# Performance work log

Hardware: AMD Instinct MI355X
Metric: run time of the kernel (lower is better)

Reference implementation:

```python
import jax, jax.numpy as jnp
import numpy as np

C = 512
B, Q, H, W = 4, 4, 64, 64


def setup_inputs() -> dict:
    key = jax.random.key(0)
    ks = jax.random.split(key, 16)
    s = 1.0 / np.sqrt(C)
    sb = 1.0 / np.sqrt(C // 4)
    return {
        "x1": jax.random.normal(ks[0], (B, C, Q, H, W), jnp.float32),
        "x2": jax.random.normal(ks[1], (B, C, Q, H, W), jnp.float32),
        "Wq": jax.random.normal(ks[2], (C, C), jnp.float32) * s,
        "bq": jnp.zeros((C,), jnp.float32),
        "Wk": jax.random.normal(ks[3], (C, C), jnp.float32) * s,
        "bk": jnp.zeros((C,), jnp.float32),
        "Wv": jax.random.normal(ks[4], (C, C), jnp.float32) * s,
        "bv": jnp.zeros((C,), jnp.float32),
        "Wa1": jax.random.normal(ks[5], (C // 4, C), jnp.float32) * s,
        "ba1": jnp.zeros((C // 4,), jnp.float32),
        "Wa2": jax.random.normal(ks[6], (4, C // 4), jnp.float32) * sb,
        "ba2": jnp.zeros((4,), jnp.float32),
        "Wo": jax.random.normal(ks[7], (C, C), jnp.float32) * s,
        "bo": jnp.zeros((C,), jnp.float32),
        "gamma": jnp.ones((C,), jnp.float32),
        "beta": jnp.zeros((C,), jnp.float32),
    }


def _conv1x1(x, Wt, b):
    # shared 1x1 conv applied independently to each quaternion component
    # x: [B, Cin, Q, H, W] -> [B, Cout, Q, H, W]
    return jnp.einsum("oc,bcqhw->boqhw", Wt, x) + b[None, :, None, None, None]


def reference(x1, x2, Wq, bq, Wk, bk, Wv, bv, Wa1, ba1, Wa2, ba2, Wo, bo, gamma, beta):
    Bn, Cn, Qn, Hn, Wn = x1.shape
    G = Cn // 4  # head dim / channel groups
    q = _conv1x1(x1, Wq, bq)
    k = _conv1x1(x2, Wk, bk)
    v = _conv1x1(x2, Wv, bv)
    # angle gate: C -> C//4 -> relu -> 4, softmax over the 4 gate channels
    aw = jax.nn.softmax(_conv1x1(jax.nn.relu(_conv1x1(x1, Wa1, ba1)), Wa2, ba2), axis=1)  # [B,4,Q,H,W]
    def gate(t):
        return (t.reshape(Bn, G, 4, Qn, Hn, Wn) * aw[:, None]).reshape(Bn, Cn, Qn, Hn, Wn)
    q = gate(q)
    k = gate(k)
    S = Qn * Hn * Wn
    def heads(t):
        # [B,C,Q,H,W] -> [B, 4 heads, G, S]
        return t.reshape(Bn, G, 4, S).transpose(0, 2, 1, 3)
    qh, kh, vh = heads(q), heads(k), heads(v)
    scale = 1.0 / jnp.sqrt(jnp.asarray(G, qh.dtype))
    attn = jax.nn.softmax(jnp.einsum("bhgs,bhfs->bhgf", qh, kh) * scale, axis=-1)  # [B,4,G,G]
    out = jnp.einsum("bhgf,bhfs->bhgs", attn, vh)  # [B,4,G,S]
    out = out.transpose(0, 2, 1, 3).reshape(Bn, Cn, Qn, Hn, Wn)
    out = _conv1x1(out, Wo, bo)
    # IQBN: normalize each (channel, quaternion component) over (B,H,W)
    mean = out.mean(axis=(0, 3, 4), keepdims=True)
    var = out.var(axis=(0, 3, 4), keepdims=True)
    out = (out - mean) / jnp.sqrt(var + 1e-5)
    return out * gamma[None, :, None, None, None] + beta[None, :, None, None, None]
```

## Files before the change

### kernel.cpp

```cpp
#include <hip/hip_runtime.h>


#define DEVI __device__ __forceinline__
typedef unsigned short u16;
typedef __bf16 bf16x8 __attribute__((ext_vector_type(8)));
typedef float f32x4 __attribute__((ext_vector_type(4)));

DEVI float bf2f(unsigned int u) {
  union { unsigned int u; float f; } v; v.u = u << 16; return v.f;
}
DEVI u16 f2bf(float f) {
  union { float f; unsigned int u; } v; v.f = f;
  unsigned int r = v.u + 0x7FFFu + ((v.u >> 16) & 1u);
  return (u16)(r >> 16);
}
DEVI void gload_lds16(const void* gp, void* lp) {
  __builtin_amdgcn_global_load_lds((const __attribute__((address_space(1))) int*)gp,
                                   (__attribute__((address_space(3))) int*)lp, 16, 0, 0);
}

__global__ __launch_bounds__(256) void cvtW_k(const float* __restrict__ Wq, const float* __restrict__ Wk,
                                              const float* __restrict__ Wa1, u16* __restrict__ WQB,
                                              u16* __restrict__ WKB, u16* __restrict__ WA1B) {
  int i = blockIdx.x * 256 + threadIdx.x;
  const float* src; u16* dst; int off;
  if (i < 65536) { src = Wq; dst = WQB; off = i; }
  else if (i < 131072) { src = Wk; dst = WKB; off = i - 65536; }
  else { src = Wa1; dst = WA1B; off = i - 131072; }
  float4 v = reinterpret_cast<const float4*>(src)[off];
  ushort4 o; o.x = f2bf(v.x); o.y = f2bf(v.y); o.z = f2bf(v.z); o.w = f2bf(v.w);
  reinterpret_cast<ushort4*>(dst)[off] = o;
}

__global__ __launch_bounds__(256) void transpose_cvt(const float* __restrict__ in, u16* __restrict__ out,
                                                     int R, int Cc, long sIn, long sOut) {
  __shared__ float tile[64][65];
  const int t = threadIdx.x;
  const int c0 = blockIdx.x * 64, r0 = blockIdx.y * 64, b = blockIdx.z;
  const float* ip = in + (long)b * sIn;
  u16* op = out + (long)b * sOut;
#pragma unroll
  for (int i = 0; i < 4; ++i) {
    int r = (t >> 4) + i * 16;
    int c = (t & 15) * 4;
    float4 v = *reinterpret_cast<const float4*>(ip + (long)(r0 + r) * Cc + c0 + c);
    tile[r][c] = v.x; tile[r][c + 1] = v.y; tile[r][c + 2] = v.z; tile[r][c + 3] = v.w;
  }
  __syncthreads();
#pragma unroll
  for (int i = 0; i < 4; ++i) {
    int c = (t >> 4) + i * 16;
    int r = (t & 15) * 4;
    ushort4 o;
    o.x = f2bf(tile[r][c]); o.y = f2bf(tile[r + 1][c]);
    o.z = f2bf(tile[r + 2][c]); o.w = f2bf(tile[r + 3][c]);
    *reinterpret_cast<ushort4*>(op + (long)(c0 + c) * R + r0 + r) = o;
  }
}

__global__ __launch_bounds__(256) void woh_k(const float* __restrict__ Wo, u16* __restrict__ Woh) {
  int idx = blockIdx.x * 256 + threadIdx.x;
  int h = idx >> 16;
  int o = (idx >> 7) & 511;
  int g = idx & 127;
  union { float f; unsigned int u; } v; v.f = Wo[(long)o * 512 + 4 * g + h];
  unsigned int r = v.u + 0x7FFFu + ((v.u >> 16) & 1u);
  Woh[idx] = (u16)(r >> 16);
}

enum { MODE_GATE = 0, MODE_BIAS = 1, MODE_PLAIN = 2, MODE_FOLD1 = 3 };

template <int MODE>
__global__ __launch_bounds__(256) void gemm_bt(const u16* __restrict__ A, const u16* __restrict__ Bt,
                                               u16* __restrict__ C, const float* __restrict__ bias,
                                               const float* __restrict__ aw, float* __restrict__ stata,
                                               int M, int N, int K, long sA, long sB, long sC) {
  __shared__ union {
    struct { u16 As[128 * 64]; u16 Bs[128 * 64]; } st;
    float racc[128][2];
  } sm;
  const int t = threadIdx.x;
  const int bn = blockIdx.x, bm = blockIdx.y, bz = blockIdx.z;
  const u16* Ab; const u16* Bb;
  if constexpr (MODE == MODE_FOLD1) {
    Ab = A + (long)(bz & 3) * 512 * 128;
    Bb = Bt + (long)bz * 128 * 128;
  } else {
    Ab = A + (long)bz * sA;
    Bb = Bt + (long)bz * sB;
  }
  const u16* Atile = Ab + (long)(bm * 128) * K;
  const u16* Btile = Bb + (long)(bn * 128) * K;
  const int wid = t >> 6, l = t & 63;
  const int rbase = (wid >> 1) * 64, cbase = (wid & 1) * 64;
  const int lr = l & 15, hi = l >> 4;
  f32x4 acc[4][4] = {};
  for (int kt = 0; kt < K; kt += 64) {
#pragma unroll
    for (int i = 0; i < 4; ++i) {
      int idx = t + i * 256;
      int r = idx >> 3;
      int gs = ((idx & 7) ^ (r & 7)) * 8;
      gload_lds16(Atile + (long)r * K + kt + gs, &sm.st.As[idx * 8]);
      gload_lds16(Btile + (long)r * K + kt + gs, &sm.st.Bs[idx * 8]);
    }
    __syncthreads();
#pragma unroll
    for (int s = 0; s < 2; ++s) {
      bf16x8 av[4], bv[4];
#pragma unroll
      for (int m = 0; m < 4; ++m) {
        int ra = rbase + m * 16 + lr;
        av[m] = *reinterpret_cast<const bf16x8*>(&sm.st.As[ra * 64 + ((4 * s + hi) ^ (ra & 7)) * 8]);
      }
#pragma unroll
      for (int n = 0; n < 4; ++n) {
        int rb = cbase + n * 16 + lr;
        bv[n] = *reinterpret_cast<const bf16x8*>(&sm.st.Bs[rb * 64 + ((4 * s + hi) ^ (rb & 7)) * 8]);
      }
#pragma unroll
      for (int m = 0; m < 4; ++m)
#pragma unroll
        for (int n = 0; n < 4; ++n)
          acc[m][n] = __builtin_amdgcn_mfma_f32_16x16x32_bf16(av[m], bv[n], acc[m][n], 0, 0, 0);
    }
    __syncthreads();
  }

  int qq = 0;
  if constexpr (MODE == MODE_BIAS) {
    if (t < 128) { sm.racc[t][0] = 0.f; sm.racc[t][1] = 0.f; }
    __syncthreads();
    qq = bn >> 5;
  }
#pragma unroll
  for (int m = 0; m < 4; ++m) {
#pragma unroll
    for (int r = 0; r < 4; ++r) {
      int rloc = rbase + m * 16 + hi * 4 + r;
      int row = bm * 128 + rloc;
      float bval = 0.f;
      if constexpr (MODE == MODE_GATE) bval = bias[row];
      if constexpr (MODE == MODE_BIAS) bval = bias[bz * M + row];
      float rs = 0.f, rq = 0.f;
#pragma unroll
      for (int n = 0; n < 4; ++n) {
        int col = bn * 128 + cbase + n * 16 + lr;
        float v = acc[m][n][r] + bval;
        if constexpr (MODE == MODE_GATE) {
          v *= aw[((long)bz * 4 + (row & 3)) * N + col];
          C[((long)(bz * 4 + (row & 3)) * 128 + (row >> 2)) * 16384 + col] = f2bf(v);
        } else if constexpr (MODE == MODE_FOLD1) {
          C[((long)(bz >> 2) * 512 + row) * 512 + 4 * col + (bz & 3)] = f2bf(v);
        } else {
          C[(long)bz * sC + (long)row * N + col] = f2bf(v);
        }
        if constexpr (MODE == MODE_BIAS) { rs += v; rq += v * v; }
      }
      if constexpr (MODE == MODE_BIAS) {
        atomicAdd(&sm.racc[rloc][0], rs);
        atomicAdd(&sm.racc[rloc][1], rq);
      }
    }
  }
  if constexpr (MODE == MODE_BIAS) {
    __syncthreads();
    if (t < 128) {
      int c = bm * 128 + t;
      atomicAdd(&stata[(c * 4 + qq) * 2], sm.racc[t][0]);
      atomicAdd(&stata[(c * 4 + qq) * 2 + 1], sm.racc[t][1]);
    }
  }
}

__global__ __launch_bounds__(256) void gemm_a1_aw(const u16* __restrict__ Wa1b, const u16* __restrict__ X1t,
                                                  const float* __restrict__ ba1, const float* __restrict__ Wa2,
                                                  const float* __restrict__ ba2, float* __restrict__ AW) {
  __shared__ union {
    struct { u16 As[128 * 64]; u16 Bs[128 * 64]; } st;
    float a1s[128][129];
  } u;
  __shared__ float wa2s[512];
  const int t = threadIdx.x;
  const int bn = blockIdx.x, bz = blockIdx.z;
  for (int i = t; i < 512; i += 256) wa2s[i] = Wa2[i];
  const u16* Btile = X1t + (long)bz * 16384 * 512 + (long)(bn * 128) * 512;
  const int wid = t >> 6, l = t & 63;
  const int rbase = (wid >> 1) * 64, cbase = (wid & 1) * 64;
  const int lr = l & 15, hi = l >> 4;
  f32x4 acc[4][4] = {};
  for (int kt = 0; kt < 512; kt += 64) {
#pragma unroll
    for (int i = 0; i < 4; ++i) {
      int idx = t + i * 256;
      int r = idx >> 3;
      int gs = ((idx & 7) ^ (r & 7)) * 8;
      gload_lds16(Wa1b + (long)r * 512 + kt + gs, &u.st.As[idx * 8]);
      gload_lds16(Btile + (long)r * 512 + kt + gs, &u.st.Bs[idx * 8]);
    }
    __syncthreads();
#pragma unroll
    for (int s = 0; s < 2; ++s) {
      bf16x8 av[4], bv[4];
#pragma unroll
      for (int m = 0; m < 4; ++m) {
        int ra = rbase + m * 16 + lr;
        av[m] = *reinterpret_cast<const bf16x8*>(&u.st.As[ra * 64 + ((4 * s + hi) ^ (ra & 7)) * 8]);
      }
#pragma unroll
      for (int n = 0; n < 4; ++n) {
        int rb = cbase + n * 16 + lr;
        bv[n] = *reinterpret_cast<const bf16x8*>(&u.st.Bs[rb * 64 + ((4 * s + hi) ^ (rb & 7)) * 8]);
      }
#pragma unroll
      for (int m = 0; m < 4; ++m)
#pragma unroll
        for (int n = 0; n < 4; ++n)
          acc[m][n] = __builtin_amdgcn_mfma_f32_16x16x32_bf16(av[m], bv[n], acc[m][n], 0, 0, 0);
    }
    __syncthreads();
  }
#pragma unroll
  for (int m = 0; m < 4; ++m) {
#pragma unroll
    for (int r = 0; r < 4; ++r) {
      int row = rbase + m * 16 + hi * 4 + r;
      float bval = ba1[row];
#pragma unroll
      for (int n = 0; n < 4; ++n) {
        int col = cbase + n * 16 + lr;
        float v = acc[m][n][r] + bval;
        u.a1s[col][row] = v > 0.f ? v : 0.f;
      }
    }
  }
  __syncthreads();
  if (t < 128) {
    float a0 = ba2[0], a1 = ba2[1], a2 = ba2[2], a3 = ba2[3];
#pragma unroll 4
    for (int c = 0; c < 128; ++c) {
      float av = u.a1s[t][c];
      a0 += wa2s[c] * av; a1 += wa2s[128 + c] * av;
      a2 += wa2s[256 + c] * av; a3 += wa2s[384 + c] * av;
    }
    float mx = fmaxf(fmaxf(a0, a1), fmaxf(a2, a3));
    float e0 = __expf(a0 - mx), e1 = __expf(a1 - mx), e2 = __expf(a2 - mx), e3 = __expf(a3 - mx);
    float inv = 1.f / (e0 + e1 + e2 + e3);
    long sg = (long)bn * 128 + t;
    float* awp = AW + (long)bz * 4 * 16384;
    awp[sg] = e0 * inv;
    awp[16384 + sg] = e1 * inv;
    awp[2 * 16384 + sg] = e2 * inv;
    awp[3 * 16384 + sg] = e3 * inv;
  }
}

__global__ __launch_bounds__(256) void logits_k(const u16* __restrict__ Qh, const u16* __restrict__ Kh,
                                                float* __restrict__ Lp) {
  __shared__ u16 As[128 * 64];
  __shared__ u16 Bs[128 * 64];
  const long S = 16384;
  const int ks = blockIdx.x;
  const int bh = blockIdx.y;
  const int t = threadIdx.x;
  const int wid = t >> 6, l = t & 63;
  const int rbase = (wid >> 1) * 64, cbase = (wid & 1) * 64;
  const int lr = l & 15, hi = l >> 4;
  const u16* qb = Qh + (long)bh * 128 * S + ks * 512;
  const u16* kb = Kh + (long)bh * 128 * S + ks * 512;
  f32x4 acc[4][4] = {};
  for (int kt = 0; kt < 512; kt += 64) {
#pragma unroll
    for (int i = 0; i < 4; ++i) {
      int idx = t + i * 256;
      int r = idx >> 3;
      int gs = ((idx & 7) ^ (r & 7)) * 8;
      gload_lds16(qb + (long)r * S + kt + gs, &As[idx * 8]);
      gload_lds16(kb + (long)r * S + kt + gs, &Bs[idx * 8]);
    }
    __syncthreads();
#pragma unroll
    for (int s = 0; s < 2; ++s) {
      bf16x8 av[4], bv[4];
#pragma unroll
      for (int m = 0; m < 4; ++m) {
        int ra = rbase + m * 16 + lr;
        av[m] = *reinterpret_cast<const bf16x8*>(&As[ra * 64 + ((4 * s + hi) ^ (ra & 7)) * 8]);
      }
#pragma unroll
      for (int n = 0; n < 4; ++n) {
        int rb = cbase + n * 16 + lr;
        bv[n] = *reinterpret_cast<const bf16x8*>(&Bs[rb * 64 + ((4 * s + hi) ^ (rb & 7)) * 8]);
      }
#pragma unroll
      for (int m = 0; m < 4; ++m)
#pragma unroll
        for (int n = 0; n < 4; ++n)
          acc[m][n] = __builtin_amdgcn_mfma_f32_16x16x32_bf16(av[m], bv[n], acc[m][n], 0, 0, 0);
    }
    __syncthreads();
  }
  float* Lb = Lp + ((long)ks * 16 + bh) * 16384;
#pragma unroll
  for (int m = 0; m < 4; ++m)
#pragma unroll
    for (int r = 0; r < 4; ++r) {
      int row = rbase + m * 16 + hi * 4 + r;
#pragma unroll
      for (int n = 0; n < 4; ++n) {
        int col = cbase + n * 16 + lr;
        Lb[row * 128 + col] = acc[m][n][r];
      }
    }
}

__global__ __launch_bounds__(256) void softmax_attnT(const float* __restrict__ Lp, u16* __restrict__ attnT) {
  const float scale = 0.08838834764831845f;
  int row = blockIdx.x * 4 + (threadIdx.x >> 6);
  int l = threadIdx.x & 63;
  int bh = row >> 7, g = row & 127;
  const float* base = Lp + (long)bh * 16384 + (long)g * 128;
  float v0 = 0.f, v1 = 0.f;
#pragma unroll 4
  for (int sp = 0; sp < 32; ++sp) {
    v0 += base[(long)sp * 16 * 16384 + l];
    v1 += base[(long)sp * 16 * 16384 + l + 64];
  }
  v0 *= scale; v1 *= scale;
  float m = fmaxf(v0, v1);
  for (int off = 32; off; off >>= 1) m = fmaxf(m, __shfl_xor(m, off));
  float e0 = __expf(v0 - m), e1 = __expf(v1 - m);
  float s = e0 + e1;
  for (int off = 32; off; off >>= 1) s += __shfl_xor(s, off);
  float inv = 1.f / s;
  u16* at = attnT + (long)bh * 16384 + g;
  at[(long)l * 128] = f2bf(e0 * inv);
  at[(long)(l + 64) * 128] = f2bf(e1 * inv);
}

__global__ __launch_bounds__(256) void b2_k(const u16* __restrict__ Weff, const float* __restrict__ bv,
                                            const float* __restrict__ bo, float* __restrict__ b2) {
  int idx = blockIdx.x * 256 + threadIdx.x;
  int b = idx >> 9, o = idx & 511;
  const u16* w = Weff + ((long)b * 512 + o) * 512;
  float s = bo[o];
  for (int c = 0; c < 512; ++c) s += bf2f(w[c]) * bv[c];
  b2[idx] = s;
}

__global__ __launch_bounds__(256) void norm_k(const u16* __restrict__ o2, const float* __restrict__ stata,
                                              const float* __restrict__ gamma, const float* __restrict__ beta,
                                              float* __restrict__ out) {
  long i8 = ((long)blockIdx.x * 256 + threadIdx.x) * 8;
  int c = (int)((i8 >> 14) & 511);
  int s = (int)(i8 & 16383);
  int g0 = c * 4 + (s >> 12);
  float sum = stata[g0 * 2], sq = stata[g0 * 2 + 1];
  float mean = sum * (1.f / 16384.f);
  float var = sq * (1.f / 16384.f) - mean * mean;
  float inv = rsqrtf(var + 1e-5f);
  float sc = inv * gamma[c];
  float sh = beta[c] - mean * sc;
  uint4 v = *reinterpret_cast<const uint4*>(o2 + i8);
  const unsigned int* pv = reinterpret_cast<const unsigned int*>(&v);
  float4 ra, rb;
  ra.x = bf2f(pv[0] & 0xffffu) * sc + sh; ra.y = bf2f(pv[0] >> 16) * sc + sh;
  ra.z = bf2f(pv[1] & 0xffffu) * sc + sh; ra.w = bf2f(pv[1] >> 16) * sc + sh;
  rb.x = bf2f(pv[2] & 0xffffu) * sc + sh; rb.y = bf2f(pv[2] >> 16) * sc + sh;
  rb.z = bf2f(pv[3] & 0xffffu) * sc + sh; rb.w = bf2f(pv[3] >> 16) * sc + sh;
  *reinterpret_cast<float4*>(out + i8) = ra;
  *reinterpret_cast<float4*>(out + i8 + 4) = rb;
}

extern "C" void kernel_launch(void* const* d_in, const int* in_sizes, int n_in,
                              void* d_out, int out_size, void* d_ws, size_t ws_size,
                              hipStream_t stream) {
  const float* x1 = (const float*)d_in[0];
  const float* x2 = (const float*)d_in[1];
  const float* Wq = (const float*)d_in[2];
  const float* bq = (const float*)d_in[3];
  const float* Wk = (const float*)d_in[4];
  const float* bk = (const float*)d_in[5];
  const float* Wv = (const float*)d_in[6];
  const float* bv = (const float*)d_in[7];
  const float* Wa1 = (const float*)d_in[8];
  const float* ba1 = (const float*)d_in[9];
  const float* Wa2 = (const float*)d_in[10];
  const float* ba2 = (const float*)d_in[11];
  const float* Wo = (const float*)d_in[12];
  const float* bo = (const float*)d_in[13];
  const float* gamma = (const float*)d_in[14];
  const float* beta = (const float*)d_in[15];
  float* out = (float*)d_out;

  char* ws = (char*)d_ws;
  const long MB = 1024L * 1024L;
  u16* X1T = (u16*)(ws);
  u16* X2T = (u16*)(ws + 64 * MB);
  u16* Qh  = (u16*)(ws + 128 * MB);
  u16* Kh  = (u16*)(ws + 192 * MB);
  float* AW = (float*)(ws + 256 * MB);
  float* STATA = (float*)(ws + 257 * MB);
  u16* ATT  = (u16*)(ws + 258 * MB);
  u16* WEFF = (u16*)(ws + 259 * MB);
  u16* W2   = (u16*)(ws + 261 * MB);
  u16* WQB  = (u16*)(ws + 263 * MB);
  u16* WKB  = (u16*)(ws + 263 * MB + 512 * 1024);
  u16* WA1B = (u16*)(ws + 264 * MB);
  u16* WVT  = (u16*)(ws + 264 * MB + 256 * 1024);
  u16* WOH  = (u16*)(ws + 264 * MB + 768 * 1024);
  float* B2 = (float*)(ws + 265 * MB + 256 * 1024);
  float* Lp = (float*)(ws);
  u16* O2 = X1T;
  (void)ws_size; (void)in_sizes; (void)n_in; (void)out_size;

  dim3 blk(256);
  const long SC = (long)16384 * 512;

  cvtW_k<<<dim3(576), blk, 0, stream>>>(Wq, Wk, Wa1, WQB, WKB, WA1B);
  woh_k<<<dim3(1024), blk, 0, stream>>>(Wo, WOH);
  transpose_cvt<<<dim3(8, 8, 1), blk, 0, stream>>>(Wv, WVT, 512, 512, 0, 0);
  transpose_cvt<<<dim3(256, 8, 4), blk, 0, stream>>>(x1, X1T, 512, 16384, SC, SC);
  transpose_cvt<<<dim3(256, 8, 4), blk, 0, stream>>>(x2, X2T, 512, 16384, SC, SC);
  hipMemsetAsync(STATA, 0, 2048 * 2 * sizeof(float), stream);

  gemm_a1_aw<<<dim3(128, 1, 4), blk, 0, stream>>>(WA1B, X1T, ba1, Wa2, ba2, AW);

  gemm_bt<MODE_GATE><<<dim3(128, 4, 4), blk, 0, stream>>>(WQB, X1T, Qh, bq, AW, nullptr,
                                                          512, 16384, 512, 0L, SC, SC);
  gemm_bt<MODE_GATE><<<dim3(128, 4, 4), blk, 0, stream>>>(WKB, X2T, Kh, bk, AW, nullptr,
                                                          512, 16384, 512, 0L, SC, SC);

  logits_k<<<dim3(32, 16), blk, 0, stream>>>(Qh, Kh, Lp);
  softmax_attnT<<<dim3(512), blk, 0, stream>>>(Lp, ATT);

  gemm_bt<MODE_FOLD1><<<dim3(1, 4, 16), blk, 0, stream>>>(WOH, ATT, WEFF, nullptr, nullptr, nullptr,
                                                          512, 128, 128, 0L, 0L, 0L);
  b2_k<<<dim3(8), blk, 0, stream>>>(WEFF, bv, bo, B2);
  gemm_bt<MODE_PLAIN><<<dim3(4, 4, 4), blk, 0, stream>>>(WEFF, WVT, W2, nullptr, nullptr, nullptr,
                                                         512, 512, 512, 512L * 512L, 0L, 512L * 512L);

  gemm_bt<MODE_BIAS><<<dim3(128, 4, 4), blk, 0, stream>>>(W2, X2T, O2, B2, nullptr, STATA,
                                                          512, 16384, 512, 512L * 512L, SC, SC);

  norm_k<<<dim3(16384), blk, 0, stream>>>(O2, STATA, gamma, beta, out);
}
```

Baseline: 847.5 us.

## Pre-swizzle bf16 operands in global memory so GEMM tile loads are contiguous

```diff
diff --git a/kernel.cpp b/kernel.cpp
--- a/kernel.cpp
+++ b/kernel.cpp
@@ -29,7 +29,10 @@
   else { src = Wa1; dst = WA1B; off = i - 131072; }
   float4 v = reinterpret_cast<const float4*>(src)[off];
   ushort4 o; o.x = f2bf(v.x); o.y = f2bf(v.y); o.z = f2bf(v.z); o.w = f2bf(v.w);
-  reinterpret_cast<ushort4*>(dst)[off] = o;
+  int e0 = off * 4;
+  int row = e0 >> 9, c = e0 & 511;
+  int cs = c ^ ((row & 7) << 3);
+  reinterpret_cast<ushort4*>(dst)[(row * 512 + cs) >> 2] = o;
 }
 
 __global__ __launch_bounds__(256) void transpose_cvt(const float* __restrict__ in, u16* __restrict__ out,
@@ -54,7 +57,9 @@
     ushort4 o;
     o.x = f2bf(tile[r][c]); o.y = f2bf(tile[r + 1][c]);
     o.z = f2bf(tile[r + 2][c]); o.w = f2bf(tile[r + 3][c]);
-    *reinterpret_cast<ushort4*>(op + (long)(c0 + c) * R + r0 + r) = o;
+    int orow = c0 + c;
+    int ic = (r0 + r) ^ ((orow & 7) << 3);
+    *reinterpret_cast<ushort4*>(op + (long)orow * R + ic) = o;
   }
 }
 
@@ -65,7 +70,8 @@
   int g = idx & 127;
   union { float f; unsigned int u; } v; v.f = Wo[(long)o * 512 + 4 * g + h];
   unsigned int r = v.u + 0x7FFFu + ((v.u >> 16) & 1u);
-  Woh[idx] = (u16)(r >> 16);
+  int gs = g ^ ((o & 7) << 3);
+  Woh[(h << 16) + (o << 7) + gs] = (u16)(r >> 16);
 }
 
 enum { MODE_GATE = 0, MODE_BIAS = 1, MODE_PLAIN = 2, MODE_FOLD1 = 3 };
@@ -100,9 +106,8 @@
     for (int i = 0; i < 4; ++i) {
       int idx = t + i * 256;
       int r = idx >> 3;
-      int gs = ((idx & 7) ^ (r & 7)) * 8;
-      gload_lds16(Atile + (long)r * K + kt + gs, &sm.st.As[idx * 8]);
-      gload_lds16(Btile + (long)r * K + kt + gs, &sm.st.Bs[idx * 8]);
+      gload_lds16(Atile + (long)r * K + kt + (idx & 7) * 8, &sm.st.As[idx * 8]);
+      gload_lds16(Btile + (long)r * K + kt + (idx & 7) * 8, &sm.st.Bs[idx * 8]);
     }
     __syncthreads();
 #pragma unroll
@@ -149,9 +154,14 @@
         float v = acc[m][n][r] + bval;
         if constexpr (MODE == MODE_GATE) {
           v *= aw[((long)bz * 4 + (row & 3)) * N + col];
-          C[((long)(bz * 4 + (row & 3)) * 128 + (row >> 2)) * 16384 + col] = f2bf(v);
+          int g = row >> 2;
+          int scol = col ^ ((g & 7) << 3);
+          C[((long)(bz * 4 + (row & 3)) * 128 + g) * 16384 + scol] = f2bf(v);
         } else if constexpr (MODE == MODE_FOLD1) {
-          C[((long)(bz >> 2) * 512 + row) * 512 + 4 * col + (bz & 3)] = f2bf(v);
+          int cp = (4 * col + (bz & 3)) ^ ((row & 7) << 3);
+          C[((long)(bz >> 2) * 512 + row) * 512 + cp] = f2bf(v);
+        } else if constexpr (MODE == MODE_PLAIN) {
+          C[(long)bz * sC + (long)row * N + (col ^ ((row & 7) << 3))] = f2bf(v);
         } else {
           C[(long)bz * sC + (long)row * N + col] = f2bf(v);
         }
@@ -194,9 +204,8 @@
     for (int i = 0; i < 4; ++i) {
       int idx = t + i * 256;
       int r = idx >> 3;
-      int gs = ((idx & 7) ^ (r & 7)) * 8;
-      gload_lds16(Wa1b + (long)r * 512 + kt + gs, &u.st.As[idx * 8]);
-      gload_lds16(Btile + (long)r * 512 + kt + gs, &u.st.Bs[idx * 8]);
+      gload_lds16(Wa1b + (long)r * 512 + kt + (idx & 7) * 8, &u.st.As[idx * 8]);
+      gload_lds16(Btile + (long)r * 512 + kt + (idx & 7) * 8, &u.st.Bs[idx * 8]);
     }
     __syncthreads();
 #pragma unroll
@@ -274,9 +283,8 @@
     for (int i = 0; i < 4; ++i) {
       int idx = t + i * 256;
       int r = idx >> 3;
-      int gs = ((idx & 7) ^ (r & 7)) * 8;
-      gload_lds16(qb + (long)r * S + kt + gs, &As[idx * 8]);
-      gload_lds16(kb + (long)r * S + kt + gs, &Bs[idx * 8]);
+      gload_lds16(qb + (long)r * S + kt + (idx & 7) * 8, &As[idx * 8]);
+      gload_lds16(kb + (long)r * S + kt + (idx & 7) * 8, &Bs[idx * 8]);
     }
     __syncthreads();
 #pragma unroll
@@ -333,9 +341,10 @@
   float s = e0 + e1;
   for (int off = 32; off; off >>= 1) s += __shfl_xor(s, off);
   float inv = 1.f / s;
-  u16* at = attnT + (long)bh * 16384 + g;
-  at[(long)l * 128] = f2bf(e0 * inv);
-  at[(long)(l + 64) * 128] = f2bf(e1 * inv);
+  u16* at = attnT + (long)bh * 16384;
+  int gs = g ^ ((l & 7) << 3);
+  at[(long)l * 128 + gs] = f2bf(e0 * inv);
+  at[(long)(l + 64) * 128 + gs] = f2bf(e1 * inv);
 }
 
 __global__ __launch_bounds__(256) void b2_k(const u16* __restrict__ Weff, const float* __restrict__ bv,
@@ -343,8 +352,9 @@
   int idx = blockIdx.x * 256 + threadIdx.x;
   int b = idx >> 9, o = idx & 511;
   const u16* w = Weff + ((long)b * 512 + o) * 512;
+  int xk = (o & 7) << 3;
   float s = bo[o];
-  for (int c = 0; c < 512; ++c) s += bf2f(w[c]) * bv[c];
+  for (int c = 0; c < 512; ++c) s += bf2f(w[c ^ xk]) * bv[c];
   b2[idx] = s;
 }
 
```

Result: slower. 870.7 us (+2.7%).
